# Kernel optimization log

Hardware: AMD Instinct MI355X
Metric: run time of the kernel (lower is better)

## Reference

```python
import jax, jax.numpy as jnp
import numpy as np
from jax import lax

B, C, H, W = 4, 256, 64, 64
C8 = C // 8  # 32


def setup_inputs() -> dict:
    key = jax.random.key(0)
    ks = jax.random.split(key, 8)
    x = jax.random.normal(ks[0], (B, C, H, W), jnp.float32)
    # 1x1 conv weights stored as [out_ch, in_ch]
    wb = jax.random.normal(ks[1], (C8, 2 * C), jnp.float32) * 0.02
    bb = jax.random.normal(ks[2], (C8,), jnp.float32) * 0.02
    wc = jax.random.normal(ks[3], (C8, 2 * C), jnp.float32) * 0.02
    bc = jax.random.normal(ks[4], (C8,), jnp.float32) * 0.02
    wd = jax.random.normal(ks[5], (C, 2 * C), jnp.float32) * 0.02
    bd = jax.random.normal(ks[6], (C,), jnp.float32) * 0.02
    alpha = jnp.float32(0.5)  # nn.Parameter(zeros(1)) at init; nonzero for a meaningful test
    return {"x": x, "wb": wb, "bb": bb, "wc": wc, "bc": bc, "wd": wd, "bd": bd, "alpha": alpha}


def reference(x, wb, bb, wc, bc, wd, bd, alpha):
    b, c, h, w = x.shape
    n = h * w
    pad = [(0, 0), (0, 0), (1, 1), (1, 1)]
    # F.avg_pool2d(k=3, s=1, p=1) with count_include_pad=True -> window-sum / 9
    x_avg = lax.reduce_window(x, 0.0, lax.add, (1, 1, 3, 3), (1, 1, 1, 1), pad) / 9.0
    x_max = lax.reduce_window(x, -jnp.inf, lax.max, (1, 1, 3, 3), (1, 1, 1, 1), pad)
    cat = jnp.concatenate([x_avg, x_max], axis=1)  # [B, 2C, H, W]
    catf = cat.reshape(b, 2 * c, n)                # [B, 2C, N]
    # 1x1 convs == per-pixel linear projections
    feat_b = jnp.einsum('oc,bcn->bon', wb, catf) + bb[None, :, None]  # [B, C8, N]
    feat_c = jnp.einsum('oc,bcn->bon', wc, catf) + bc[None, :, None]  # [B, C8, N]
    feat_d = jnp.einsum('oc,bcn->bon', wd, catf) + bd[None, :, None]  # [B, C,  N]
    # attention_s = softmax(feat_b^T @ feat_c) over last dim -> [B, N, N]
    attn = jax.nn.softmax(jnp.einsum('bon,bom->bnm', feat_b, feat_c), axis=-1)
    # feat_e = feat_d @ attn^T -> [B, C, N]
    feat_e = jnp.einsum('bcn,bmn->bcm', feat_d, attn).reshape(b, c, h, w)
    return alpha * feat_e + (1.0 - alpha) * x
```

## Files before the change

### kernel.cpp

```cpp
#include <hip/hip_runtime.h>
#include <hip/hip_bf16.h>

typedef __hip_bfloat16 bf16;
typedef __attribute__((ext_vector_type(8))) short s8v;
typedef __attribute__((ext_vector_type(4))) float f4v;

__device__ __forceinline__ ushort f2u(float f) {
    bf16 h = __float2bfloat16(f);
    return *(ushort*)&h;
}


__global__ __launch_bounds__(256) void pool_kernel(
    const float* __restrict__ x, ushort* __restrict__ cat,
    const float* __restrict__ wb, const float* __restrict__ wc,
    const float* __restrict__ wd, ushort* __restrict__ Wf) {
    int bid = blockIdx.x;
    int tid = threadIdx.x;
    if (bid >= 1024) {
        int f = (bid - 1024) * 4 + (tid >> 6);
        int l = tid & 63;
        int ot = f % 20, kc = f / 20;
        int o = ot * 16 + (l & 15);
        int k0 = kc * 32 + (l >> 4) * 8;
        const float* wr = (o < 32) ? wb + (size_t)o * 512
                        : (o < 64) ? wc + (size_t)(o - 32) * 512
                                   : wd + (size_t)(o - 64) * 512;
        float4 f0 = *(const float4*)(wr + k0);
        float4 f1 = *(const float4*)(wr + k0 + 4);
        ushort tmp[8] = {f2u(f0.x), f2u(f0.y), f2u(f0.z), f2u(f0.w),
                         f2u(f1.x), f2u(f1.y), f2u(f1.z), f2u(f1.w)};
        *(uint4*)(Wf + kc * 10240 + ot * 512 + l * 8) = *(uint4*)tmp;
        return;
    }
    __shared__ float Xs[3][64][66];
    int b = bid >> 8, h = (bid >> 2) & 63, cg = bid & 3;
    bool hasU = (h > 0), hasD = (h < 63);
    #pragma unroll
    for (int pp = 0; pp < 12; ++pp) {
        int linear = pp * 256 + tid;
        int w4 = linear & 15;
        int cs = (linear >> 4) & 63;
        int dh = linear >> 10;
        int hh = h + dh - 1;
        float4 f = {0.f, 0.f, 0.f, 0.f};
        if ((unsigned)hh < 64u)
            f = *(const float4*)(x + ((size_t)(b * 256 + cg * 64 + cs)) * 4096
                                 + hh * 64 + w4 * 4);
        Xs[dh][w4 * 4 + 0][cs] = f.x;
        Xs[dh][w4 * 4 + 1][cs] = f.y;
        Xs[dh][w4 * 4 + 2][cs] = f.z;
        Xs[dh][w4 * 4 + 3][cs] = f.w;
    }
    __syncthreads();
    int cs = tid & 63, ws = tid >> 6;
    float vs[18], vm[18];
    #pragma unroll
    for (int j = 0; j < 18; ++j) {
        int w = ws * 16 - 1 + j;
        if ((unsigned)w < 64u) {
            float u = Xs[0][w][cs], m = Xs[1][w][cs], d = Xs[2][w][cs];
            vs[j] = u + m + d;
            float mx = m;
            if (hasU) mx = fmaxf(mx, u);
            if (hasD) mx = fmaxf(mx, d);
            vm[j] = mx;
        } else { vs[j] = 0.f; vm[j] = -3.4e38f; }
    }
    size_t nb = ((size_t)b * 4096 + h * 64 + ws * 16) * 512 + cg * 64 + cs;
    #pragma unroll
    for (int i = 0; i < 16; ++i) {
        float sum = vs[i] + vs[i + 1] + vs[i + 2];
        float mx  = fmaxf(fmaxf(vm[i], vm[i + 1]), vm[i + 2]);
        cat[nb + (size_t)i * 512]       = f2u(sum * (1.f / 9.f));
        cat[nb + (size_t)i * 512 + 256] = f2u(mx);
    }
}

__global__ __launch_bounds__(256, 2) void proj_kernel(
    const ushort* __restrict__ cat, const ushort* __restrict__ Wf,
    const float* __restrict__ bb, const float* __restrict__ bc,
    const float* __restrict__ bd,
    ushort* __restrict__ Qb, ushort* __restrict__ Kb, ushort* __restrict__ Vf) {
    __shared__ __align__(16) ushort As[32][72];
    __shared__ __align__(16) ushort Vls[256][40];
    int tid = threadIdx.x;
    int l = tid & 63, w = tid >> 6;
    int lm = l & 15, q = l >> 4;
    int n0 = blockIdx.x * 32;
    f4v acc[2][5];
    #pragma unroll
    for (int mt = 0; mt < 2; ++mt)
        #pragma unroll
        for (int ot = 0; ot < 5; ++ot)
            #pragma unroll
            for (int i = 0; i < 4; ++i) acc[mt][ot][i] = 0.f;

    const ushort* wfb = Wf + (w * 5) * 512 + l * 8;
    int sr = tid >> 3, sko = (tid & 7) * 8;
    const ushort* srow = cat + (size_t)(n0 + sr) * 512 + sko;

    for (int kc = 0; kc < 8; ++kc) {
        *(uint4*)&As[sr][sko] = *(const uint4*)(srow + kc * 64);
        __syncthreads();
        #pragma unroll
        for (int ks = 0; ks < 2; ++ks) {
            int kci = kc * 2 + ks;
            s8v bf[5];
            #pragma unroll
            for (int ot = 0; ot < 5; ++ot)
                bf[ot] = *(const s8v*)(wfb + kci * 10240 + ot * 512);
            s8v a0 = *(const s8v*)&As[lm][ks * 32 + q * 8];
            s8v a1 = *(const s8v*)&As[16 + lm][ks * 32 + q * 8];
            #pragma unroll
            for (int ot = 0; ot < 5; ++ot) {
                acc[0][ot] = __builtin_amdgcn_mfma_f32_16x16x32_bf16(a0, bf[ot], acc[0][ot], 0, 0, 0);
                acc[1][ot] = __builtin_amdgcn_mfma_f32_16x16x32_bf16(a1, bf[ot], acc[1][ot], 0, 0, 0);
            }
        }
        __syncthreads();
    }
    #pragma unroll
    for (int ot = 0; ot < 5; ++ot) {
        int o = w * 80 + ot * 16 + lm;
        if (o < 32) {
            float bias = bb[o];
            #pragma unroll
            for (int mt = 0; mt < 2; ++mt)
                #pragma unroll
                for (int r = 0; r < 4; ++r)
                    Qb[(size_t)(n0 + mt * 16 + q * 4 + r) * 32 + o]
                        = f2u(acc[mt][ot][r] + bias);
        } else if (o < 64) {
            float bias = bc[o - 32];
            #pragma unroll
            for (int mt = 0; mt < 2; ++mt)
                #pragma unroll
                for (int r = 0; r < 4; ++r)
                    Kb[(size_t)(n0 + mt * 16 + q * 4 + r) * 32 + (o - 32)]
                        = f2u(acc[mt][ot][r] + bias);
        } else {
            int c = o - 64;
            float bias = bd[c];
            #pragma unroll
            for (int mt = 0; mt < 2; ++mt) {
                ushort tmp[4];
                #pragma unroll
                for (int r = 0; r < 4; ++r) tmp[r] = f2u(acc[mt][ot][r] + bias);
                *(uint2*)&Vls[c][mt * 16 + q * 4] = *(uint2*)tmp;
            }
        }
    }
    __syncthreads();
    {
        int bidx = n0 >> 12;
        size_t fb = ((size_t)bidx << 20) + (size_t)((n0 & 4095) >> 5) * 8192 + l * 8;
        #pragma unroll
        for (int i = 0; i < 4; ++i) {
            int cb = w * 4 + i;
            *(uint4*)(Vf + fb + cb * 512) = *(const uint4*)&Vls[cb * 16 + lm][q * 8];
        }
    }
}

__global__ __launch_bounds__(512, 2) void attn_kernel(
    const ushort* __restrict__ Qb, const ushort* __restrict__ Kb,
    const ushort* __restrict__ Vf, const float* __restrict__ x,
    const float* __restrict__ alphap, float* __restrict__ out) {
    __shared__ __align__(16) ushort Ps[2][64][72];
    __shared__ float Obuf[4][64][17];
    __shared__ float Lpart[4][64];
    __shared__ float Lrow[64];
    int tid = threadIdx.x;
    int l = tid & 63, w = tid >> 6;
    int lm = l & 15, q = l >> 4;
    int nsw = w & 3, kh = w >> 2;
    int bid = blockIdx.x;
    int xcd = bid & 7;
    int b = xcd & 3;
    int midx = (bid >> 3) + ((xcd >> 2) << 5);
    int m0 = midx << 6;
    size_t bN = (size_t)b << 12;

    s8v Qf[2];
    {
        const ushort* qb = Qb + (bN + m0 + kh * 32) * 32;
        Qf[0] = *(const s8v*)(qb + (size_t)(lm) * 32 + q * 8);
        Qf[1] = *(const s8v*)(qb + (size_t)(16 + lm) * 32 + q * 8);
    }
    const ushort* kbp = Kb + (bN + nsw * 16 + lm) * 32 + q * 8;
    const ushort* vfp = Vf + ((size_t)b << 20) + kh * 8192 + (nsw * 4) * 512 + l * 8;

    f4v acc[4][4];
    #pragma unroll
    for (int mt = 0; mt < 4; ++mt)
        #pragma unroll
        for (int ct = 0; ct < 4; ++ct)
            #pragma unroll
            for (int i = 0; i < 4; ++i) acc[mt][ct][i] = 0.f;
    float La0 = 0.f, La1 = 0.f;

    s8v kf0 = *(const s8v*)kbp;
    s8v kf1 = *(const s8v*)(kbp + 2048);
    s8v vfA[4], vfB[4];
    #pragma unroll
    for (int ct = 0; ct < 4; ++ct) vfA[ct] = *(const s8v*)(vfp + ct * 512);
    {
        f4v S0 = {0.f, 0.f, 0.f, 0.f}, S1 = {0.f, 0.f, 0.f, 0.f};
        S0 = __builtin_amdgcn_mfma_f32_16x16x32_bf16(kf0, Qf[0], S0, 0, 0, 0);
        S1 = __builtin_amdgcn_mfma_f32_16x16x32_bf16(kf0, Qf[1], S1, 0, 0, 0);
        ushort e0[4], e1[4];
        #pragma unroll
        for (int r = 0; r < 4; ++r) {
            float f0 = __expf(fminf(S0[r], 60.f));
            float f1 = __expf(fminf(S1[r], 60.f));
            La0 += f0; La1 += f1;
            e0[r] = f2u(f0); e1[r] = f2u(f1);
        }
        *(uint2*)&Ps[0][kh * 32 + lm][nsw * 16 + q * 4]      = *(uint2*)e0;
        *(uint2*)&Ps[0][kh * 32 + 16 + lm][nsw * 16 + q * 4] = *(uint2*)e1;
    }
    __syncthreads();

#define TILE_BODY(TT, KFS, KFP, VCUR, VNXT)                                       \
    {                                                                             \
        int p = (TT) & 1;                                                         \
        if ((TT) < 62) KFP = *(const s8v*)(kbp + (size_t)((TT) + 2) * 2048);      \
        if ((TT) < 63) {                                                          \
            const ushort* vn = vfp + (size_t)((TT) + 1) * 16384;                  \
            _Pragma("unroll")                                                     \
            for (int ct = 0; ct < 4; ++ct)                                        \
                VNXT[ct] = *(const s8v*)(vn + ct * 512);                          \
        }                                                                         \
        f4v S0 = {0.f, 0.f, 0.f, 0.f}, S1 = {0.f, 0.f, 0.f, 0.f};                 \
        if ((TT) < 63) {                                                          \
            S0 = __builtin_amdgcn_mfma_f32_16x16x32_bf16(KFS, Qf[0], S0, 0, 0, 0);\
            S1 = __builtin_amdgcn_mfma_f32_16x16x32_bf16(KFS, Qf[1], S1, 0, 0, 0);\
        }                                                                         \
        s8v Af0 = *(const s8v*)&Ps[p][lm][kh * 32 + q * 8];                       \
        s8v Af1 = *(const s8v*)&Ps[p][16 + lm][kh * 32 + q * 8];                  \
        s8v Af2 = *(const s8v*)&Ps[p][32 + lm][kh * 32 + q * 8];                  \
        s8v Af3 = *(const s8v*)&Ps[p][48 + lm][kh * 32 + q * 8];                  \
        if ((TT) < 63) {                                                          \
            ushort e0[4], e1[4];                                                  \
            _Pragma("unroll")                                                     \
            for (int r = 0; r < 4; ++r) {                                         \
                float f0 = __expf(fminf(S0[r], 60.f));                            \
                float f1 = __expf(fminf(S1[r], 60.f));                            \
                La0 += f0; La1 += f1;                                             \
                e0[r] = f2u(f0); e1[r] = f2u(f1);                                 \
            }                                                                     \
            *(uint2*)&Ps[1 - p][kh * 32 + lm][nsw * 16 + q * 4]      = *(uint2*)e0;\
            *(uint2*)&Ps[1 - p][kh * 32 + 16 + lm][nsw * 16 + q * 4] = *(uint2*)e1;\
        }                                                                         \
        _Pragma("unroll")                                                         \
        for (int ct = 0; ct < 4; ++ct) {                                          \
            acc[0][ct] = __builtin_amdgcn_mfma_f32_16x16x32_bf16(Af0, VCUR[ct], acc[0][ct], 0, 0, 0); \
            acc[1][ct] = __builtin_amdgcn_mfma_f32_16x16x32_bf16(Af1, VCUR[ct], acc[1][ct], 0, 0, 0); \
            acc[2][ct] = __builtin_amdgcn_mfma_f32_16x16x32_bf16(Af2, VCUR[ct], acc[2][ct], 0, 0, 0); \
            acc[3][ct] = __builtin_amdgcn_mfma_f32_16x16x32_bf16(Af3, VCUR[ct], acc[3][ct], 0, 0, 0); \
        }                                                                         \
        asm volatile("s_waitcnt lgkmcnt(0)\n\ts_barrier" ::: "memory");           \
    }

    for (int t = 0; t < 64; t += 2) {
        TILE_BODY(t,     kf1, kf0, vfA, vfB);
        TILE_BODY(t + 1, kf0, kf1, vfB, vfA);
    }
#undef TILE_BODY

    La0 += __shfl_xor(La0, 16, 64); La0 += __shfl_xor(La0, 32, 64);
    La1 += __shfl_xor(La1, 16, 64); La1 += __shfl_xor(La1, 32, 64);
    if (q == 0) {
        Lpart[nsw][kh * 32 + lm]      = La0;
        Lpart[nsw][kh * 32 + 16 + lm] = La1;
    }
    __syncthreads();
    if (tid < 64)
        Lrow[tid] = Lpart[0][tid] + Lpart[1][tid] + Lpart[2][tid] + Lpart[3][tid];
    __syncthreads();
    #pragma unroll
    for (int ct = 0; ct < 4; ++ct) {
        if (kh == 1) {
            #pragma unroll
            for (int mt = 0; mt < 4; ++mt)
                #pragma unroll
                for (int r = 0; r < 4; ++r)
                    Obuf[nsw][mt * 16 + q * 4 + r][lm] = acc[mt][ct][r];
        }
        __syncthreads();
        if (kh == 0) {
            #pragma unroll
            for (int mt = 0; mt < 4; ++mt)
                #pragma unroll
                for (int r = 0; r < 4; ++r)
                    acc[mt][ct][r] += Obuf[nsw][mt * 16 + q * 4 + r][lm];
        }
        __syncthreads();
    }
    if (kh == 0) {
        float alpha = alphap[0];
        float ra = 1.f - alpha;
        #pragma unroll
        for (int mt = 0; mt < 4; ++mt) {
            float L0 = Lrow[mt * 16 + q * 4 + 0];
            float L1 = Lrow[mt * 16 + q * 4 + 1];
            float L2 = Lrow[mt * 16 + q * 4 + 2];
            float L3 = Lrow[mt * 16 + q * 4 + 3];
            #pragma unroll
            for (int ct = 0; ct < 4; ++ct) {
                int cc = nsw * 64 + ct * 16 + lm;
                size_t base = ((size_t)(b * 256 + cc)) * 4096 + m0 + mt * 16 + q * 4;
                float4 xv = *(const float4*)(x + base);
                float4 ov;
                ov.x = alpha * (acc[mt][ct][0] / L0) + ra * xv.x;
                ov.y = alpha * (acc[mt][ct][1] / L1) + ra * xv.y;
                ov.z = alpha * (acc[mt][ct][2] / L2) + ra * xv.z;
                ov.w = alpha * (acc[mt][ct][3] / L3) + ra * xv.w;
                *(float4*)(out + base) = ov;
            }
        }
    }
}

extern "C" void kernel_launch(void* const* d_in, const int* in_sizes, int n_in,
                              void* d_out, int out_size, void* d_ws, size_t ws_size,
                              hipStream_t stream) {
    const float* x  = (const float*)d_in[0];
    const float* wb = (const float*)d_in[1];
    const float* bb = (const float*)d_in[2];
    const float* wc = (const float*)d_in[3];
    const float* bc = (const float*)d_in[4];
    const float* wd = (const float*)d_in[5];
    const float* bd = (const float*)d_in[6];
    const float* al = (const float*)d_in[7];
    float* out = (float*)d_out;

    char* ws = (char*)d_ws;
    ushort* cat = (ushort*)ws;
    ushort* Qb  = (ushort*)(ws + 16777216);
    ushort* Kb  = (ushort*)(ws + 17825792);
    ushort* Vf  = (ushort*)(ws + 18874368);
    ushort* Wf  = (ushort*)(ws + 27262976);

    pool_kernel<<<dim3(1104), dim3(256), 0, stream>>>(x, cat, wb, wc, wd, Wf);
    proj_kernel<<<dim3(512), dim3(256), 0, stream>>>(cat, Wf, bb, bc, bd,
                                                     Qb, Kb, Vf);
    attn_kernel<<<dim3(256), dim3(512), 0, stream>>>(Qb, Kb, Vf, x, al, out);
}
```

Measured before the change: 167.0 us.

## Fuse pooling and projection into one kernel keeping pooled features in LDS

Merges the pooling kernel and the 1x1 projection kernel into a single kernel. Each block handles one image row: it pools all 256 channels into shared memory, prefetching the next channel group's input into registers while the current group is pooled, then runs the MFMA projection straight from shared memory. This removes the 16 MB bf16 concatenated-feature buffer round trip through global memory. The weight conversion moves to its own small kernel. In exchange the fused kernel uses about 117 KB of shared memory per block, which limits occupancy, and the projection phase now launches only 256 blocks.

```diff
diff --git a/kernel.cpp b/kernel.cpp
--- a/kernel.cpp
+++ b/kernel.cpp
@@ -11,154 +11,173 @@
 }
 
 
-__global__ __launch_bounds__(256) void pool_kernel(
-    const float* __restrict__ x, ushort* __restrict__ cat,
+__global__ __launch_bounds__(256) void wcvt_kernel(
     const float* __restrict__ wb, const float* __restrict__ wc,
     const float* __restrict__ wd, ushort* __restrict__ Wf) {
-    int bid = blockIdx.x;
-    int tid = threadIdx.x;
-    if (bid >= 1024) {
-        int f = (bid - 1024) * 4 + (tid >> 6);
-        int l = tid & 63;
-        int ot = f % 20, kc = f / 20;
-        int o = ot * 16 + (l & 15);
-        int k0 = kc * 32 + (l >> 4) * 8;
-        const float* wr = (o < 32) ? wb + (size_t)o * 512
-                        : (o < 64) ? wc + (size_t)(o - 32) * 512
-                                   : wd + (size_t)(o - 64) * 512;
-        float4 f0 = *(const float4*)(wr + k0);
-        float4 f1 = *(const float4*)(wr + k0 + 4);
-        ushort tmp[8] = {f2u(f0.x), f2u(f0.y), f2u(f0.z), f2u(f0.w),
-                         f2u(f1.x), f2u(f1.y), f2u(f1.z), f2u(f1.w)};
-        *(uint4*)(Wf + kc * 10240 + ot * 512 + l * 8) = *(uint4*)tmp;
-        return;
-    }
-    __shared__ float Xs[3][64][66];
-    int b = bid >> 8, h = (bid >> 2) & 63, cg = bid & 3;
-    bool hasU = (h > 0), hasD = (h < 63);
-    #pragma unroll
-    for (int pp = 0; pp < 12; ++pp) {
-        int linear = pp * 256 + tid;
-        int w4 = linear & 15;
-        int cs = (linear >> 4) & 63;
-        int dh = linear >> 10;
-        int hh = h + dh - 1;
-        float4 f = {0.f, 0.f, 0.f, 0.f};
-        if ((unsigned)hh < 64u)
-            f = *(const float4*)(x + ((size_t)(b * 256 + cg * 64 + cs)) * 4096
-                                 + hh * 64 + w4 * 4);
-        Xs[dh][w4 * 4 + 0][cs] = f.x;
-        Xs[dh][w4 * 4 + 1][cs] = f.y;
-        Xs[dh][w4 * 4 + 2][cs] = f.z;
-        Xs[dh][w4 * 4 + 3][cs] = f.w;
-    }
-    __syncthreads();
-    int cs = tid & 63, ws = tid >> 6;
-    float vs[18], vm[18];
-    #pragma unroll
-    for (int j = 0; j < 18; ++j) {
-        int w = ws * 16 - 1 + j;
-        if ((unsigned)w < 64u) {
-            float u = Xs[0][w][cs], m = Xs[1][w][cs], d = Xs[2][w][cs];
-            vs[j] = u + m + d;
-            float mx = m;
-            if (hasU) mx = fmaxf(mx, u);
-            if (hasD) mx = fmaxf(mx, d);
-            vm[j] = mx;
-        } else { vs[j] = 0.f; vm[j] = -3.4e38f; }
-    }
-    size_t nb = ((size_t)b * 4096 + h * 64 + ws * 16) * 512 + cg * 64 + cs;
-    #pragma unroll
-    for (int i = 0; i < 16; ++i) {
-        float sum = vs[i] + vs[i + 1] + vs[i + 2];
-        float mx  = fmaxf(fmaxf(vm[i], vm[i + 1]), vm[i + 2]);
-        cat[nb + (size_t)i * 512]       = f2u(sum * (1.f / 9.f));
-        cat[nb + (size_t)i * 512 + 256] = f2u(mx);
-    }
-}
-
-__global__ __launch_bounds__(256, 2) void proj_kernel(
-    const ushort* __restrict__ cat, const ushort* __restrict__ Wf,
+    int f = blockIdx.x * 4 + (threadIdx.x >> 6);
+    int l = threadIdx.x & 63;
+    int ot = f % 20, kc = f / 20;
+    int o = ot * 16 + (l & 15);
+    int k0 = kc * 32 + (l >> 4) * 8;
+    const float* wr = (o < 32) ? wb + (size_t)o * 512
+                    : (o < 64) ? wc + (size_t)(o - 32) * 512
+                               : wd + (size_t)(o - 64) * 512;
+    float4 f0 = *(const float4*)(wr + k0);
+    float4 f1 = *(const float4*)(wr + k0 + 4);
+    ushort tmp[8] = {f2u(f0.x), f2u(f0.y), f2u(f0.z), f2u(f0.w),
+                     f2u(f1.x), f2u(f1.y), f2u(f1.z), f2u(f1.w)};
+    *(uint4*)(Wf + kc * 10240 + ot * 512 + l * 8) = *(uint4*)tmp;
+}
+
+__global__ __launch_bounds__(512, 2) void fused_kernel(
+    const float* __restrict__ x, const ushort* __restrict__ Wf,
     const float* __restrict__ bb, const float* __restrict__ bc,
     const float* __restrict__ bd,
     ushort* __restrict__ Qb, ushort* __restrict__ Kb, ushort* __restrict__ Vf) {
-    __shared__ __align__(16) ushort As[32][72];
-    __shared__ __align__(16) ushort Vls[256][40];
+    __shared__ __align__(16) char smem[117248];
+    float*  Xs   = (float*)smem;
+    ushort* Vls  = (ushort*)smem;
+    ushort* catS = (ushort*)(smem + 50688);
+
     int tid = threadIdx.x;
+    int bid = blockIdx.x;
+    int lb = (bid & 7) * 32 + (bid >> 3);
+    int b = lb >> 6, h = lb & 63;
+    bool hasU = (h > 0), hasD = (h < 63);
+
+    float4 xr[6];
+#define LOADCG(CG)                                                              \
+    {                                                                           \
+        _Pragma("unroll")                                                       \
+        for (int pp = 0; pp < 6; ++pp) {                                        \
+            int linear = pp * 512 + tid;                                        \
+            int w4 = linear & 15, cs_s = (linear >> 4) & 63, dh = linear >> 10; \
+            int hh = h + dh - 1;                                                \
+            float4 fv = {0.f, 0.f, 0.f, 0.f};                                   \
+            if ((unsigned)hh < 64u)                                             \
+                fv = *(const float4*)(x + ((size_t)(b * 256 + (CG) * 64 + cs_s)) * 4096 \
+                                      + hh * 64 + w4 * 4);                      \
+            xr[pp] = fv;                                                        \
+        }                                                                       \
+    }
+    LOADCG(0)
+    #pragma unroll
+    for (int cg = 0; cg < 4; ++cg) {
+        #pragma unroll
+        for (int pp = 0; pp < 6; ++pp) {
+            int linear = pp * 512 + tid;
+            int w4 = linear & 15, cs_s = (linear >> 4) & 63, dh = linear >> 10;
+            float* xp = Xs + (dh * 64 + w4 * 4) * 66 + cs_s;
+            xp[0]   = xr[pp].x;
+            xp[66]  = xr[pp].y;
+            xp[132] = xr[pp].z;
+            xp[198] = xr[pp].w;
+        }
+        __syncthreads();
+        if (cg == 0) LOADCG(1)
+        else if (cg == 1) LOADCG(2)
+        else if (cg == 2) LOADCG(3)
+        {
+            int cs = tid & 63, wsw = tid >> 6;
+            float vs[10], vm[10];
+            #pragma unroll
+            for (int j = 0; j < 10; ++j) {
+                int w = wsw * 8 - 1 + j;
+                if ((unsigned)w < 64u) {
+                    float u = Xs[w * 66 + cs];
+                    float m = Xs[(64 + w) * 66 + cs];
+                    float d = Xs[(128 + w) * 66 + cs];
+                    vs[j] = u + m + d;
+                    float mx = m;
+                    if (hasU) mx = fmaxf(mx, u);
+                    if (hasD) mx = fmaxf(mx, d);
+                    vm[j] = mx;
+                } else { vs[j] = 0.f; vm[j] = -3.4e38f; }
+            }
+            int chb = cg * 64 + cs;
+            #pragma unroll
+            for (int i = 0; i < 8; ++i) {
+                float sum = vs[i] + vs[i + 1] + vs[i + 2];
+                float mx  = fmaxf(fmaxf(vm[i], vm[i + 1]), vm[i + 2]);
+                catS[(wsw * 8 + i) * 520 + chb]       = f2u(sum * (1.f / 9.f));
+                catS[(wsw * 8 + i) * 520 + 256 + chb] = f2u(mx);
+            }
+        }
+        __syncthreads();
+    }
+#undef LOADCG
+
     int l = tid & 63, w = tid >> 6;
     int lm = l & 15, q = l >> 4;
-    int n0 = blockIdx.x * 32;
-    f4v acc[2][5];
-    #pragma unroll
-    for (int mt = 0; mt < 2; ++mt)
-        #pragma unroll
-        for (int ot = 0; ot < 5; ++ot)
-            #pragma unroll
-            for (int i = 0; i < 4; ++i) acc[mt][ot][i] = 0.f;
-
-    const ushort* wfb = Wf + (w * 5) * 512 + l * 8;
-    int sr = tid >> 3, sko = (tid & 7) * 8;
-    const ushort* srow = cat + (size_t)(n0 + sr) * 512 + sko;
-
-    for (int kc = 0; kc < 8; ++kc) {
-        *(uint4*)&As[sr][sko] = *(const uint4*)(srow + kc * 64);
-        __syncthreads();
-        #pragma unroll
-        for (int ks = 0; ks < 2; ++ks) {
-            int kci = kc * 2 + ks;
-            s8v bf[5];
-            #pragma unroll
-            for (int ot = 0; ot < 5; ++ot)
-                bf[ot] = *(const s8v*)(wfb + kci * 10240 + ot * 512);
-            s8v a0 = *(const s8v*)&As[lm][ks * 32 + q * 8];
-            s8v a1 = *(const s8v*)&As[16 + lm][ks * 32 + q * 8];
-            #pragma unroll
-            for (int ot = 0; ot < 5; ++ot) {
-                acc[0][ot] = __builtin_amdgcn_mfma_f32_16x16x32_bf16(a0, bf[ot], acc[0][ot], 0, 0, 0);
-                acc[1][ot] = __builtin_amdgcn_mfma_f32_16x16x32_bf16(a1, bf[ot], acc[1][ot], 0, 0, 0);
-            }
-        }
-        __syncthreads();
-    }
-    #pragma unroll
-    for (int ot = 0; ot < 5; ++ot) {
-        int o = w * 80 + ot * 16 + lm;
-        if (o < 32) {
+    int nc = w & 3, oh = w >> 2;
+    f4v pacc[10];
+    #pragma unroll
+    for (int ot = 0; ot < 10; ++ot)
+        #pragma unroll
+        for (int i = 0; i < 4; ++i) pacc[ot][i] = 0.f;
+
+    const ushort* wfp = Wf + (oh * 10) * 512 + l * 8;
+    const ushort* ap  = catS + (nc * 16 + lm) * 520 + q * 8;
+    #pragma unroll 2
+    for (int kci = 0; kci < 16; ++kci) {
+        s8v Af = *(const s8v*)(ap + kci * 32);
+        s8v Bf[10];
+        #pragma unroll
+        for (int ot = 0; ot < 10; ++ot)
+            Bf[ot] = *(const s8v*)(wfp + kci * 10240 + ot * 512);
+        #pragma unroll
+        for (int ot = 0; ot < 10; ++ot)
+            pacc[ot] = __builtin_amdgcn_mfma_f32_16x16x32_bf16(Af, Bf[ot], pacc[ot], 0, 0, 0);
+    }
+
+    size_t nrow = (size_t)((b << 12) + h * 64 + nc * 16 + q * 4);
+    if (oh == 0) {
+        #pragma unroll
+        for (int ot = 0; ot < 2; ++ot) {
+            int o = ot * 16 + lm;
             float bias = bb[o];
             #pragma unroll
-            for (int mt = 0; mt < 2; ++mt)
-                #pragma unroll
-                for (int r = 0; r < 4; ++r)
-                    Qb[(size_t)(n0 + mt * 16 + q * 4 + r) * 32 + o]
-                        = f2u(acc[mt][ot][r] + bias);
-        } else if (o < 64) {
-            float bias = bc[o - 32];
-            #pragma unroll
-            for (int mt = 0; mt < 2; ++mt)
-                #pragma unroll
-                for (int r = 0; r < 4; ++r)
-                    Kb[(size_t)(n0 + mt * 16 + q * 4 + r) * 32 + (o - 32)]
-                        = f2u(acc[mt][ot][r] + bias);
-        } else {
-            int c = o - 64;
+            for (int r = 0; r < 4; ++r)
+                Qb[(nrow + r) * 32 + o] = f2u(pacc[ot][r] + bias);
+        }
+        #pragma unroll
+        for (int ot = 2; ot < 4; ++ot) {
+            int o = ot * 16 + lm - 32;
+            float bias = bc[o];
+            #pragma unroll
+            for (int r = 0; r < 4; ++r)
+                Kb[(nrow + r) * 32 + o] = f2u(pacc[ot][r] + bias);
+        }
+        #pragma unroll
+        for (int ot = 4; ot < 10; ++ot) {
+            int c = ot * 16 + lm - 64;
             float bias = bd[c];
-            #pragma unroll
-            for (int mt = 0; mt < 2; ++mt) {
-                ushort tmp[4];
-                #pragma unroll
-                for (int r = 0; r < 4; ++r) tmp[r] = f2u(acc[mt][ot][r] + bias);
-                *(uint2*)&Vls[c][mt * 16 + q * 4] = *(uint2*)tmp;
-            }
+            ushort tmp[4];
+            #pragma unroll
+            for (int r = 0; r < 4; ++r) tmp[r] = f2u(pacc[ot][r] + bias);
+            *(uint2*)&Vls[c * 72 + nc * 16 + q * 4] = *(uint2*)tmp;
+        }
+    } else {
+        #pragma unroll
+        for (int ot = 0; ot < 10; ++ot) {
+            int c = 96 + ot * 16 + lm;
+            float bias = bd[c];
+            ushort tmp[4];
+            #pragma unroll
+            for (int r = 0; r < 4; ++r) tmp[r] = f2u(pacc[ot][r] + bias);
+            *(uint2*)&Vls[c * 72 + nc * 16 + q * 4] = *(uint2*)tmp;
         }
     }
     __syncthreads();
     {
-        int bidx = n0 >> 12;
-        size_t fb = ((size_t)bidx << 20) + (size_t)((n0 & 4095) >> 5) * 8192 + l * 8;
-        #pragma unroll
-        for (int i = 0; i < 4; ++i) {
-            int cb = w * 4 + i;
-            *(uint4*)(Vf + fb + cb * 512) = *(const uint4*)&Vls[cb * 16 + lm][q * 8];
+        size_t vb = ((size_t)b << 20) + (size_t)(h * 2) * 8192 + l * 8;
+        #pragma unroll
+        for (int i = 0; i < 2; ++i) {
+            int cb = w * 2 + i;
+            #pragma unroll
+            for (int nh = 0; nh < 2; ++nh)
+                *(uint4*)(Vf + vb + nh * 8192 + cb * 512)
+                    = *(const uint4*)&Vls[(cb * 16 + lm) * 72 + nh * 32 + q * 8];
         }
     }
 }
@@ -337,14 +356,13 @@
     float* out = (float*)d_out;
 
     char* ws = (char*)d_ws;
-    ushort* cat = (ushort*)ws;
-    ushort* Qb  = (ushort*)(ws + 16777216);
-    ushort* Kb  = (ushort*)(ws + 17825792);
-    ushort* Vf  = (ushort*)(ws + 18874368);
-    ushort* Wf  = (ushort*)(ws + 27262976);
-
-    pool_kernel<<<dim3(1104), dim3(256), 0, stream>>>(x, cat, wb, wc, wd, Wf);
-    proj_kernel<<<dim3(512), dim3(256), 0, stream>>>(cat, Wf, bb, bc, bd,
-                                                     Qb, Kb, Vf);
+    ushort* Qb = (ushort*)ws;
+    ushort* Kb = (ushort*)(ws + 1048576);
+    ushort* Vf = (ushort*)(ws + 2097152);
+    ushort* Wf = (ushort*)(ws + 10485760);
+
+    wcvt_kernel<<<dim3(80), dim3(256), 0, stream>>>(wb, wc, wd, Wf);
+    fused_kernel<<<dim3(256), dim3(512), 0, stream>>>(x, Wf, bb, bc, bd,
+                                                      Qb, Kb, Vf);
     attn_kernel<<<dim3(256), dim3(512), 0, stream>>>(Qb, Kb, Vf, x, al, out);
 }
```

Measured after the change: 164.2 us. About the same (-1.7%).
